# Performance work log

Measured on AMD Instinct MI355X. Metric: run time of the kernel, lower is better.

The kernel has to match this reference:

```python
import jax, jax.numpy as jnp
from jax import lax
import numpy as np

INF = jnp.float32(1e4)  # > max possible distance sqrt(384^2+384^2); INF**2 safe in fp32


def setup_inputs() -> dict:
    key = jax.random.key(0)
    k1, k2 = jax.random.split(key)
    pred = jax.random.normal(k1, (8, 1, 384, 384), jnp.float32)
    target = jax.random.randint(k2, (8, 1, 384, 384), 0, 2, jnp.int32)
    return {"pred": pred, "target": target}


def _dist1d(zero, axis):
    """Per-line distance to nearest True in `zero`, along `axis`. zero: bool array."""
    x = jnp.moveaxis(zero, axis, 0)
    init = jnp.full(x.shape[1:], INF, jnp.float32)
    def step(c, b):
        d = jnp.minimum(jnp.where(b, 0.0, c + 1.0), INF)
        return d, d
    _, df = lax.scan(step, init, x)
    _, db = lax.scan(step, init, x[::-1])
    d = jnp.minimum(df, db[::-1])
    return jnp.moveaxis(d, 0, axis)


def _edt(nonzero):
    """Exact 2D Euclidean distance transform: for each pixel, distance to nearest
    pixel where `nonzero` is False. nonzero: bool [B,H,W]. Matches scipy edt(nonzero).
    Separable: 1D column distance, then min-plus (lower envelope) along rows."""
    d1 = _dist1d(~nonzero, axis=1)          # [B,H,W] vertical distance to nearest zero
    f = d1 * d1
    W = f.shape[-1]
    j = jnp.arange(W, dtype=f.dtype)
    def body(_, i):
        # D(.,.,i) = min_j f(.,.,j) + (i-j)^2
        return None, jnp.min(f + (i - j) ** 2, axis=-1)
    _, out = lax.scan(body, None, j)        # [W,B,H]
    return jnp.sqrt(jnp.moveaxis(out, 0, -1))  # [B,H,W]


def _loss(pred, target):
    t = target.astype(jnp.float32)
    # BCEWithLogits (mean): softplus(x) - x*t
    bce = jnp.mean(jax.nn.softplus(pred) - pred * t)
    p = jax.nn.sigmoid(pred)
    B = pred.shape[0]
    pf = p.reshape(B, -1)
    tf = t.reshape(B, -1)
    smooth = 1e-5
    dice = (2.0 * jnp.sum(pf * tf, 1) + smooth) / (jnp.sum(pf, 1) + jnp.sum(tf, 1) + smooth)
    loss1 = 0.5 * bce + (1.0 - jnp.mean(dice))
    # signed distance field from binary target (channel 0)
    pos = target[:, 0].astype(bool)         # [B,H,W]
    posdis = _edt(~pos)                     # scipy edt(negmask)
    negdis = _edt(pos)                      # scipy edt(posmask)
    sdf = posdis - negdis                   # [B,H,W]
    # faithful to torch: [B,1,H,W] * [B,H,W] broadcasts to [B,B,H,W]
    multip = jnp.abs(p - t) * jnp.abs(sdf)
    loss2 = jnp.mean(multip)
    return 0.7 * loss1 + 0.3 * 0.1 * loss2


def reference(pred, target):
    return _loss(pred, target)
```

## Files before the change

### kernel.cpp

```cpp
#include <hip/hip_runtime.h>
#include <math.h>

#define B 8
#define H 384
#define W 384
#define HW (H*W)
#define NTOT (B*HW)
#define INF_I 10000
#define NFB 192
#define NVB 48
#define NWK 256
#define CMB (NFB+NVB+NWK)
#define TOKEN 0x7E57F1A6u

#define WS_SLOT  131072
#define WS_PART2 262144
#define WS_CW    311296
#define WS_SUMA  462848

__global__ __launch_bounds__(768) void k_all(const float* __restrict__ pred,
                                             const int* __restrict__ tgt,
                                             char* __restrict__ ws,
                                             float* __restrict__ out) {
    __shared__ float lds[12][25];
    __shared__ unsigned lcw[12][384];
    __shared__ float lfp[12][412], lfn[12][412];
    __shared__ double wpart[12];
    __shared__ double sval[25];
    __shared__ double sl2[4];
    int tid = threadIdx.x, bid = blockIdx.x;
    unsigned* flags = (unsigned*)ws;
    double* part2 = (double*)(ws + WS_PART2);
    unsigned* cwG = (unsigned*)(ws + WS_CW);
    float* sumA = (float*)(ws + WS_SUMA);

    if (bid < NFB) {
        int pix = bid * 768 + tid;
        float vals[25];
        float sA = 0.f, bce = 0.f;
#pragma unroll
        for (int b = 0; b < 8; ++b) {
            float x = pred[b * HW + pix];
            int t = tgt[b * HW + pix];
            float e = __builtin_amdgcn_exp2f(fabsf(x) * -1.442695041f);
            float rc = __builtin_amdgcn_rcpf(1.f + e);
            float p = (x >= 0.f) ? rc : 1.f - rc;
            float l1p = __builtin_amdgcn_logf(1.f + e) * 0.69314718056f;
            bce += fmaxf(x, 0.f) + l1p - x * (float)t;
            vals[1 + b] = p;
            vals[9 + b] = t ? p : 0.f;
            vals[17 + b] = (float)t;
            sA += t ? 1.f - p : p;
        }
        atomicExch((unsigned*)&sumA[pix], __float_as_uint(sA));
        vals[0] = bce;
#pragma unroll
        for (int k = 0; k < 25; ++k)
#pragma unroll
            for (int o = 32; o; o >>= 1) vals[k] += __shfl_down(vals[k], o);
        int wave = tid >> 6, lane = tid & 63;
        if (lane == 0)
#pragma unroll
            for (int k = 0; k < 25; ++k) lds[wave][k] = vals[k];
        __syncthreads();
        if (tid < 25) {
            double s = 0.0;
#pragma unroll
            for (int wv = 0; wv < 12; ++wv) s += (double)lds[wv][tid];
            atomicExch((unsigned long long*)&part2[bid * 25 + tid],
                       (unsigned long long)__double_as_longlong(s));
        }
        __syncthreads();
        if (tid == 0) atomicExch(&flags[bid * 64], TOKEN);
    } else if (bid < NFB + NVB) {
        int p = bid - NFB;
        int wd = tid >> 6, wl = tid & 63;
        int b = p / 6, w = (p % 6) * 64 + wl;
        const int* colp = tgt + b * HW + w + (wd * 32) * W;
        unsigned m = 0;
#pragma unroll
        for (int i = 0; i < 32; ++i)
            m |= (colp[i * W] != 0) ? (1u << i) : 0u;
        atomicExch(&cwG[(b * 12 + wd) * 384 + w], m);
        __syncthreads();
        if (tid == 0) atomicExch(&flags[(192 + p) * 64], TOKEN);
    } else if (bid < CMB) {
        int w = bid - (NFB + NVB);
        int b = w >> 5, stripe = w & 31;
        int h0 = stripe * 12;
        if (tid < 6) {
            int line = (192 + 6 * b + tid) * 64;
            while (atomicAdd(&flags[line], 0u) != TOKEN) __builtin_amdgcn_s_sleep(8);
        }
        __syncthreads();
        {
            const unsigned* src = cwG + b * 12 * 384;
            unsigned* dst = &lcw[0][0];
            for (int i = tid; i < 12 * 384; i += 768) dst[i] = src[i];
        }
        __syncthreads();

        {
            int col = tid >> 1, pn = tid & 1;
            unsigned cwv[12];
#pragma unroll
            for (int j = 0; j < 12; ++j) {
                unsigned mm = lcw[j][col];
                cwv[j] = pn ? ~mm : mm;
            }
            int wd0 = h0 >> 5, off = h0 & 31;
            int cin = INF_I;
            {
                unsigned mm = off ? (cwv[wd0] & ((1u << off) - 1u)) : 0u;
                int j = wd0;
                while (mm == 0u && j > 0) mm = cwv[--j];
                if (mm) cin = h0 - (j * 32 + (31 - __clz(mm)));
            }
            int cinb = INF_I;
            int he = h0 + 12;
            if (he < H) {
                int j1 = he >> 5, off1 = he & 31;
                unsigned mm = cwv[j1] & (off1 ? ~((1u << off1) - 1u) : 0xFFFFFFFFu);
                int j = j1;
                while (mm == 0u && j < 11) mm = cwv[++j];
                if (mm) cinb = (j * 32 + (__ffs(mm) - 1)) - (h0 + 11);
            }
            unsigned lo = cwv[wd0];
            unsigned hi = (wd0 < 11) ? cwv[wd0 + 1] : 0u;
            unsigned long long win = ((((unsigned long long)hi) << 32) | lo) >> off;
            int df[12];
            int c = cin;
#pragma unroll
            for (int r = 0; r < 12; ++r) {
                c = ((win >> r) & 1ull) ? 0 : min(c + 1, INF_I);
                df[r] = c;
            }
            int cb = cinb;
            int s = col + (col >> 4);
#pragma unroll
            for (int r = 11; r >= 0; --r) {
                cb = ((win >> r) & 1ull) ? 0 : min(cb + 1, INF_I);
                int d = min(df[r], cb);
                float fd = (float)d;
                if (pn) lfn[r][s] = fd * fd;
                else    lfp[r][s] = fd * fd;
            }
        }
        if (tid < 6) {
            int line = (6 * stripe + tid) * 64;
            while (atomicAdd(&flags[line], 0u) != TOKEN) __builtin_amdgcn_s_sleep(8);
        }
        __syncthreads();

        int wv = tid >> 6, lane = tid & 63;
        int h = h0 + wv;
        int base = 6 * lane - 8;
        float rp[22], rn[22];
#pragma unroll
        for (int r = 0; r < 22; ++r) {
            int j = base + r;
            j = j < 0 ? 0 : (j > W - 1 ? W - 1 : j);
            int s = j + (j >> 4);
            rp[r] = lfp[wv][s];
            rn[r] = lfn[wv][s];
        }
        const float DD[17] = {64.f,49.f,36.f,25.f,16.f,9.f,4.f,1.f,0.f,
                              1.f,4.f,9.f,16.f,25.f,36.f,49.f,64.f};
        float partial = 0.f;
#pragma unroll
        for (int q = 0; q < 6; ++q) {
            int i = 6 * lane + q;
            float Dp = 3.0e38f, Dn = 3.0e38f;
#pragma unroll
            for (int tt = 0; tt < 17; ++tt) {
                Dp = fminf(Dp, rp[q + tt] + DD[tt]);
                Dn = fminf(Dn, rn[q + tt] + DD[tt]);
            }
            if (Dp > 64.f || Dn > 64.f) {
                float fi = (float)i;
                for (int j = 0; j < W; ++j) {
                    int s = j + (j >> 4);
                    float d = fi - (float)j;
                    Dp = fminf(Dp, fmaf(d, d, lfp[wv][s]));
                    Dn = fminf(Dn, fmaf(d, d, lfn[wv][s]));
                }
            }
            float sdf = fabsf(sqrtf(Dp) - sqrtf(Dn));
            partial += sdf * sumA[h * W + i];
        }
        double v = partial;
#pragma unroll
        for (int o = 32; o; o >>= 1) v += __shfl_down(v, o);
        if (lane == 0) wpart[wv] = v;
        __syncthreads();
        if (tid == 0) {
            double bp = 0.0;
#pragma unroll
            for (int k = 0; k < 12; ++k) bp += wpart[k];
            atomicExch((unsigned long long*)(ws + WS_SLOT + w * 256),
                       (unsigned long long)__double_as_longlong(bp));
            asm volatile("s_waitcnt vmcnt(0)" ::: "memory");
            atomicExch(&flags[(240 + w) * 64], TOKEN);
        }
    } else {
        if (tid < 448) {
            int line = (tid < 192) ? tid * 64 : (240 + (tid - 192)) * 64;
            while (atomicAdd(&flags[line], 0u) != TOKEN) __builtin_amdgcn_s_sleep(8);
        }
        __syncthreads();
        if (tid < 200) {
            int v = tid >> 3, sub = tid & 7;
            double s = 0.0;
            for (int blk = sub; blk < NFB; blk += 8) s += part2[blk * 25 + v];
#pragma unroll
            for (int o = 4; o; o >>= 1) s += __shfl_down(s, o, 8);
            if (sub == 0) sval[v] = s;
        }
        double s2 = 0.0;
        if (tid < 256)
            s2 = *(const double*)(ws + WS_SLOT + tid * 256);
#pragma unroll
        for (int o = 32; o; o >>= 1) s2 += __shfl_down(s2, o);
        if (tid < 256 && (tid & 63) == 0) sl2[tid >> 6] = s2;
        __syncthreads();
        if (tid == 0) {
            double bce = sval[0] / (double)NTOT;
            double dsum = 0.0;
            for (int bb = 0; bb < 8; ++bb)
                dsum += (2.0 * sval[9 + bb] + 1e-5) / (sval[1 + bb] + sval[17 + bb] + 1e-5);
            double dice = dsum / 8.0;
            double loss1 = 0.5 * bce + (1.0 - dice);
            double loss2 = (sl2[0] + sl2[1] + sl2[2] + sl2[3])
                         / ((double)B * (double)B * (double)HW);
            out[0] = (float)(0.7 * loss1 + 0.03 * loss2);
        }
    }
}

extern "C" void kernel_launch(void* const* d_in, const int* in_sizes, int n_in,
                              void* d_out, int out_size, void* d_ws, size_t ws_size,
                              hipStream_t stream) {
    const float* pred = (const float*)d_in[0];
    const int* tgt = (const int*)d_in[1];
    float* out = (float*)d_out;
    char* ws = (char*)d_ws;

    k_all<<<CMB + 1, 768, 0, stream>>>(pred, tgt, ws, out);
}
```

Measured before the change: 21.15 us.

## Defer worker flag wait past EDT compute and derive target counts via popcount

Worker blocks now compute their per-pixel SDF values before waiting on the elementwise blocks' readiness flags. That overlaps the distance-transform work with the BCE/sigmoid blocks instead of stalling on them first. The per-batch target count is no longer reduced by the elementwise blocks; the final block computes it with popcount over the already-built column bitmasks. The final block also waits only on the worker flags and relies on them transitively covering the elementwise blocks. The sumA stores are packed two per 64-bit atomic, which halves the number of store operations but adds a cross-lane shuffle.

New measurement: 23.49 us. +11.1%, slower.

```diff
diff --git a/kernel.cpp b/kernel.cpp
--- a/kernel.cpp
+++ b/kernel.cpp
@@ -28,6 +28,7 @@
     __shared__ double wpart[12];
     __shared__ double sval[25];
     __shared__ double sl2[4];
+    __shared__ int tsum[8];
     int tid = threadIdx.x, bid = blockIdx.x;
     unsigned* flags = (unsigned*)ws;
     double* part2 = (double*)(ws + WS_PART2);
@@ -36,7 +37,7 @@
 
     if (bid < NFB) {
         int pix = bid * 768 + tid;
-        float vals[25];
+        float vals[17];
         float sA = 0.f, bce = 0.f;
 #pragma unroll
         for (int b = 0; b < 8; ++b) {
@@ -49,21 +50,27 @@
             bce += fmaxf(x, 0.f) + l1p - x * (float)t;
             vals[1 + b] = p;
             vals[9 + b] = t ? p : 0.f;
-            vals[17 + b] = (float)t;
             sA += t ? 1.f - p : p;
         }
-        atomicExch((unsigned*)&sumA[pix], __float_as_uint(sA));
+        {
+            float nxt = __shfl_down(sA, 1);
+            if ((tid & 1) == 0) {
+                unsigned long long pk = ((unsigned long long)__float_as_uint(nxt) << 32)
+                                      | (unsigned long long)__float_as_uint(sA);
+                atomicExch((unsigned long long*)&sumA[pix], pk);
+            }
+        }
         vals[0] = bce;
 #pragma unroll
-        for (int k = 0; k < 25; ++k)
+        for (int k = 0; k < 17; ++k)
 #pragma unroll
             for (int o = 32; o; o >>= 1) vals[k] += __shfl_down(vals[k], o);
         int wave = tid >> 6, lane = tid & 63;
         if (lane == 0)
 #pragma unroll
-            for (int k = 0; k < 25; ++k) lds[wave][k] = vals[k];
-        __syncthreads();
-        if (tid < 25) {
+            for (int k = 0; k < 17; ++k) lds[wave][k] = vals[k];
+        __syncthreads();
+        if (tid < 17) {
             double s = 0.0;
 #pragma unroll
             for (int wv = 0; wv < 12; ++wv) s += (double)lds[wv][tid];
@@ -146,10 +153,6 @@
                 else    lfp[r][s] = fd * fd;
             }
         }
-        if (tid < 6) {
-            int line = (6 * stripe + tid) * 64;
-            while (atomicAdd(&flags[line], 0u) != TOKEN) __builtin_amdgcn_s_sleep(8);
-        }
         __syncthreads();
 
         int wv = tid >> 6, lane = tid & 63;
@@ -166,7 +169,7 @@
         }
         const float DD[17] = {64.f,49.f,36.f,25.f,16.f,9.f,4.f,1.f,0.f,
                               1.f,4.f,9.f,16.f,25.f,36.f,49.f,64.f};
-        float partial = 0.f;
+        float sdf6[6];
 #pragma unroll
         for (int q = 0; q < 6; ++q) {
             int i = 6 * lane + q;
@@ -185,9 +188,18 @@
                     Dn = fminf(Dn, fmaf(d, d, lfn[wv][s]));
                 }
             }
-            float sdf = fabsf(sqrtf(Dp) - sqrtf(Dn));
-            partial += sdf * sumA[h * W + i];
-        }
+            sdf6[q] = fabsf(sqrtf(Dp) - sqrtf(Dn));
+        }
+        if (tid < 6) {
+            int line = (6 * stripe + tid) * 64;
+            while (atomicAdd(&flags[line], 0u) != TOKEN) __builtin_amdgcn_s_sleep(8);
+        }
+        __syncthreads();
+
+        float partial = 0.f;
+#pragma unroll
+        for (int q = 0; q < 6; ++q)
+            partial += sdf6[q] * sumA[h * W + 6 * lane + q];
         double v = partial;
 #pragma unroll
         for (int o = 32; o; o >>= 1) v += __shfl_down(v, o);
@@ -203,12 +215,21 @@
             atomicExch(&flags[(240 + w) * 64], TOKEN);
         }
     } else {
-        if (tid < 448) {
-            int line = (tid < 192) ? tid * 64 : (240 + (tid - 192)) * 64;
+        if (tid < 256) {
+            int line = (240 + tid) * 64;
             while (atomicAdd(&flags[line], 0u) != TOKEN) __builtin_amdgcn_s_sleep(8);
         }
-        __syncthreads();
-        if (tid < 200) {
+        if (tid < 8) tsum[tid] = 0;
+        __syncthreads();
+        {
+            int b = tid / 96, idx = tid % 96;
+            const unsigned* base = cwG + b * 4608 + idx * 48;
+            int s = 0;
+#pragma unroll 8
+            for (int i = 0; i < 48; ++i) s += __popc(base[i]);
+            atomicAdd(&tsum[b], s);
+        }
+        if (tid < 136) {
             int v = tid >> 3, sub = tid & 7;
             double s = 0.0;
             for (int blk = sub; blk < NFB; blk += 8) s += part2[blk * 25 + v];
@@ -227,7 +248,8 @@
             double bce = sval[0] / (double)NTOT;
             double dsum = 0.0;
             for (int bb = 0; bb < 8; ++bb)
-                dsum += (2.0 * sval[9 + bb] + 1e-5) / (sval[1 + bb] + sval[17 + bb] + 1e-5);
+                dsum += (2.0 * sval[9 + bb] + 1e-5)
+                      / (sval[1 + bb] + (double)tsum[bb] + 1e-5);
             double dice = dsum / 8.0;
             double loss1 = 0.5 * bce + (1.0 - dice);
             double loss2 = (sl2[0] + sl2[1] + sl2[2] + sl2[3])
```
